# Optimization experiments

Measured on AMD Instinct MI355X. Metric: run time of the kernel, lower is better.

The kernel has to match this reference:

```python
import jax, jax.numpy as jnp
import numpy as np

N, E, F_IN, H0, H1 = 50000, 800000, 128, 128, 64


def setup_inputs() -> dict:
    key = jax.random.key(0)
    k1, k2, k3, k4, k5, k6 = jax.random.split(key, 6)
    node_features = jax.random.normal(k1, (N, F_IN), dtype=jnp.float32)
    edges = jax.random.randint(k2, (E, 2), 0, N, dtype=jnp.int64)
    # GCNConv params (glorot-ish scale)
    W1 = jax.random.normal(k3, (F_IN, H0), dtype=jnp.float32) / np.sqrt(F_IN)
    b1 = jnp.zeros((H0,), dtype=jnp.float32)
    W2 = jax.random.normal(k4, (H0, H1), dtype=jnp.float32) / np.sqrt(H0)
    b2 = jnp.zeros((H1,), dtype=jnp.float32)
    return {"node_features": node_features, "edges": edges,
            "W1": W1, "b1": b1, "W2": W2, "b2": b2}


def reference(node_features, edges, W1, b1, W2, b2):
    # GCNConv: out = D^{-1/2} (A + I) D^{-1/2} (X W) + b, with self-loops.
    n = node_features.shape[0]
    ei = edges.T  # [2, E] like edge_index.t() in the torch code
    self_idx = jnp.arange(n, dtype=ei.dtype)
    src = jnp.concatenate([ei[0], self_idx])  # [E+N]
    dst = jnp.concatenate([ei[1], self_idx])  # [E+N]
    deg = jnp.zeros((n,), node_features.dtype).at[dst].add(1.0)  # >=1 (self-loops)
    dinv = jax.lax.rsqrt(deg)
    norm = (dinv[src] * dinv[dst])[:, None]  # [E+N, 1]

    def gcn(x, W, b):
        h = x @ W                      # dense transform [n, d_out]
        msg = h[src] * norm            # gather + scale  [E+N, d_out]
        agg = jax.ops.segment_sum(msg, dst, num_segments=n)  # scatter-add
        return agg + b

    x = jax.nn.relu(gcn(node_features, W1, b1))
    # F.dropout(training=self.training): identity in eval mode (deterministic ref)
    x = gcn(x, W2, b2)
    return x
```

## Files before the change

kernel.cpp:

```cpp
#include <hip/hip_runtime.h>
#include <hip/hip_bf16.h>


#define NCHUNK 128

#define OFF_ROWSTART (size_t)0x0
#define OFF_DINV     (size_t)0x40000
#define OFF_BLOCKSUM (size_t)0x80000
#define OFF_FLAG     (size_t)0x80800
#define OFF_LRANK    (size_t)0x81000
#define OFF_CSR      (size_t)0x150000
#define OFF_H        (size_t)0x300000
#define OFF_W1T      (size_t)0xA00000
#define OFF_W2T      (size_t)0xA10000
#define OFF_BUFA     (size_t)0xB00000
#define OFF_BUFB     (size_t)0x1800000

typedef short bf16x8 __attribute__((ext_vector_type(8)));
typedef float f32x4 __attribute__((ext_vector_type(4)));

__device__ __forceinline__ float2 bf2f(unsigned u) {
    float2 r;
    r.x = __uint_as_float(u << 16);
    r.y = __uint_as_float(u & 0xffff0000u);
    return r;
}
__device__ __forceinline__ unsigned f2bf(float a, float b) {
    __hip_bfloat162 h = __float22bfloat162_rn(make_float2(a, b));
    union { __hip_bfloat162 h; unsigned u; } cv;
    cv.h = h;
    return cv.u;
}

__global__ __launch_bounds__(256) void k_hist(const int* __restrict__ e32, int E,
                                              int chunk, int n,
                                              unsigned char* __restrict__ lrank,
                                              unsigned char* __restrict__ H,
                                              int* __restrict__ flag,
                                              const float* __restrict__ W1,
                                              const float* __restrict__ W2,
                                              unsigned short* __restrict__ W1T,
                                              unsigned short* __restrict__ W2T) {
    const int t = threadIdx.x, b = blockIdx.x;
    if (b >= NCHUNK) {
        const int bb = b - NCHUNK;
        const int k0 = (t & 15) * 8;
        if (bb < 8) {
            int nn = bb * 16 + (t >> 4);
            float w[8];
#pragma unroll
            for (int j = 0; j < 8; ++j) w[j] = W1[(size_t)(k0 + j) * 128 + nn];
            uint4 q;
            q.x = f2bf(w[0], w[1]); q.y = f2bf(w[2], w[3]);
            q.z = f2bf(w[4], w[5]); q.w = f2bf(w[6], w[7]);
            *reinterpret_cast<uint4*>(&W1T[(size_t)nn * 128 + k0]) = q;
        } else {
            int nn = (bb - 8) * 16 + (t >> 4);
            float w[8];
#pragma unroll
            for (int j = 0; j < 8; ++j) w[j] = W2[(size_t)(k0 + j) * 64 + nn];
            uint4 q;
            q.x = f2bf(w[0], w[1]); q.y = f2bf(w[2], w[3]);
            q.z = f2bf(w[4], w[5]); q.w = f2bf(w[6], w[7]);
            *reinterpret_cast<uint4*>(&W2T[(size_t)nn * 128 + k0]) = q;
        }
        return;
    }
    __shared__ unsigned h[12544];
    __shared__ int anyv;
    const int nw = (n + 3) >> 2;
    if (t == 0) anyv = 0;
    for (int i = t; i < nw; i += 256) h[i] = 0u;
    __syncthreads();
    const int e0 = b * chunk, e1 = min(E, e0 + chunk);
    int v = 0;
    const int lim = min(e1, e0 + 2048);
    for (int e = e0 + t; e < lim; e += 256) v |= e32[2 * e + 1];
    if (v) atomicOr(&anyv, 1);
    __syncthreads();
    const int f = (anyv == 0) ? 1 : 0;
    if (b == 0 && t == 0) *flag = f;
    for (int e = e0 + t; e < e1; e += 256) {
        int dst;
        if (f) dst = reinterpret_cast<const int4*>(e32)[e].z;
        else   dst = reinterpret_cast<const int2*>(e32)[e].y;
        int sh = (dst & 3) << 3;
        unsigned old = atomicAdd(&h[dst >> 2], 1u << sh);
        lrank[e] = (unsigned char)((old >> sh) & 0xffu);
    }
    __syncthreads();
    unsigned* Hp = reinterpret_cast<unsigned*>(H);
    const size_t wbase = (size_t)b * (size_t)(n >> 2);
    for (int i = t; i < (n >> 2); i += 256) Hp[wbase + i] = h[i];
}

__global__ __launch_bounds__(256) void k_mergescan(
        unsigned char* __restrict__ H, int n,
        float* __restrict__ dinv, int* __restrict__ rowstart,
        int* __restrict__ blocksum) {
    __shared__ int sh[256];
    const int t = threadIdx.x;
    const int bin0 = blockIdx.x * 1024 + 4 * t;
    int s0 = 0, s1 = 0, s2 = 0, s3 = 0;
    if (bin0 < n) {
        unsigned* Hp = reinterpret_cast<unsigned*>(H);
        const size_t wstride = (size_t)(n >> 2);
        const size_t widx = (size_t)(bin0 >> 2);
#pragma unroll 8
        for (int b = 0; b < NCHUNK; ++b) {
            size_t idx = (size_t)b * wstride + widx;
            unsigned w = Hp[idx];
            Hp[idx] = (unsigned)s0 | ((unsigned)s1 << 8) |
                      ((unsigned)s2 << 16) | ((unsigned)s3 << 24);
            s0 += (int)(w & 0xffu);
            s1 += (int)((w >> 8) & 0xffu);
            s2 += (int)((w >> 16) & 0xffu);
            s3 += (int)((w >> 24) & 0xffu);
        }
        float4 dv;
        dv.x = rsqrtf((float)s0 + 1.0f);
        dv.y = rsqrtf((float)s1 + 1.0f);
        dv.z = rsqrtf((float)s2 + 1.0f);
        dv.w = rsqrtf((float)s3 + 1.0f);
        *reinterpret_cast<float4*>(dinv + bin0) = dv;
    }
    int tot = s0 + s1 + s2 + s3;
    sh[t] = tot;
    __syncthreads();
    for (int off = 1; off < 256; off <<= 1) {
        int add = (t >= off) ? sh[t - off] : 0;
        __syncthreads();
        sh[t] += add;
        __syncthreads();
    }
    if (bin0 < n) {
        int ex = sh[t] - tot;
        int4 rs;
        rs.x = ex;
        rs.y = ex + s0;
        rs.z = ex + s0 + s1;
        rs.w = ex + s0 + s1 + s2;
        *reinterpret_cast<int4*>(rowstart + bin0) = rs;
    }
    if (t == 255) blocksum[blockIdx.x] = sh[255];
}

__global__ void k_scan3(int* __restrict__ rowstart, int n,
                        const int* __restrict__ blocksum, int nb, int E) {
    __shared__ int bs[65];
    int t = threadIdx.x;
    if (t < nb) bs[t + 1] = blocksum[t];
    if (t == 0) bs[0] = 0;
    __syncthreads();
    if (t == 0) {
        int s = 0;
        for (int k = 1; k <= nb; ++k) { s += bs[k]; bs[k] = s; }
    }
    __syncthreads();
    int i = blockIdx.x * 256 + t;
    if (i < n) rowstart[i] += bs[i >> 10];
    if (i == 0) rowstart[n] = E;
}

__global__ __launch_bounds__(256) void k_fill(const int* __restrict__ e32, int E,
                                              int chunk,
                                              const int* __restrict__ flag,
                                              const int* __restrict__ rowstart,
                                              const unsigned char* __restrict__ H,
                                              int n,
                                              const unsigned char* __restrict__ lrank,
                                              unsigned short* __restrict__ csr) {
    __shared__ unsigned char hs[50176];
    const int t = threadIdx.x;
    const int b = blockIdx.x >> 1;
    const int half = blockIdx.x & 1;
    {
        const uint4* src = reinterpret_cast<const uint4*>(H + (size_t)b * n);
        uint4* dst = reinterpret_cast<uint4*>(hs);
        for (int i = t; i < (n >> 4); i += 256) dst[i] = src[i];
    }
    __syncthreads();
    const int f = *flag;
    const int hchunk = chunk >> 1;
    const int e0 = b * chunk + half * hchunk;
    const int e1 = min(E, e0 + hchunk);
    for (int e = e0 + t; e < e1; e += 256) {
        int src, dst;
        if (f) { int4 v = reinterpret_cast<const int4*>(e32)[e]; src = v.x; dst = v.z; }
        else   { int2 v = reinterpret_cast<const int2*>(e32)[e]; src = v.x; dst = v.y; }
        csr[rowstart[dst] + (int)hs[dst] + (int)lrank[e]] = (unsigned short)src;
    }
}

__global__ __launch_bounds__(256) void k_gemm1m(const float* __restrict__ X,
                                                const unsigned short* __restrict__ W1T,
                                                const float* __restrict__ dinv,
                                                unsigned short* __restrict__ out,
                                                int n) {
    __shared__ unsigned short Xs[64 * 136];
    __shared__ unsigned short Ws[128 * 136];
    const int t = threadIdx.x;
    const int row0 = blockIdx.x * 64;
#pragma unroll
    for (int it = 0; it < 8; ++it) {
        int i = t + it * 256;
        int r = i >> 4, c8 = i & 15;
        *reinterpret_cast<uint4*>(&Ws[r * 136 + c8 * 8]) =
            *reinterpret_cast<const uint4*>(&W1T[(size_t)r * 128 + c8 * 8]);
    }
#pragma unroll
    for (int it = 0; it < 8; ++it) {
        int i = t + it * 256;
        int r = i >> 5, c4 = i & 31;
        int gr = row0 + r;
        float4 v = make_float4(0.f, 0.f, 0.f, 0.f);
        if (gr < n) v = *reinterpret_cast<const float4*>(&X[(size_t)gr * 128 + c4 * 4]);
        uint2 q;
        q.x = f2bf(v.x, v.y);
        q.y = f2bf(v.z, v.w);
        *reinterpret_cast<uint2*>(&Xs[r * 136 + c4 * 4]) = q;
    }
    __syncthreads();
    const int w = t >> 6, lane = t & 63;
    const int m = lane & 15, kg = lane >> 4;
    f32x4 acc[8] = {};
#pragma unroll
    for (int kt = 0; kt < 128; kt += 32) {
        bf16x8 a = *reinterpret_cast<const bf16x8*>(&Xs[(w * 16 + m) * 136 + kt + kg * 8]);
#pragma unroll
        for (int j = 0; j < 8; ++j) {
            bf16x8 bb = *reinterpret_cast<const bf16x8*>(&Ws[(j * 16 + m) * 136 + kt + kg * 8]);
            acc[j] = __builtin_amdgcn_mfma_f32_16x16x32_bf16(a, bb, acc[j], 0, 0, 0);
        }
    }
    const int rbase = row0 + w * 16 + kg * 4;
#pragma unroll
    for (int r = 0; r < 4; ++r) {
        int gr = rbase + r;
        if (gr < n) {
            float dv = dinv[gr];
#pragma unroll
            for (int j = 0; j < 8; ++j)
                out[(size_t)gr * 128 + j * 16 + m] =
                    (unsigned short)(f2bf(acc[j][r] * dv, 0.f) & 0xffffu);
        }
    }
}

__global__ __launch_bounds__(256) void k_gemm2m(const unsigned short* __restrict__ X1,
                                                const unsigned short* __restrict__ W2T,
                                                const float* __restrict__ dinv,
                                                unsigned short* __restrict__ out,
                                                int n) {
    __shared__ unsigned short Xs[64 * 136];
    __shared__ unsigned short Ws[64 * 136];
    const int t = threadIdx.x;
    const int row0 = blockIdx.x * 64;
#pragma unroll
    for (int it = 0; it < 4; ++it) {
        int i = t + it * 256;
        int r = i >> 4, c8 = i & 15;
        *reinterpret_cast<uint4*>(&Ws[r * 136 + c8 * 8]) =
            *reinterpret_cast<const uint4*>(&W2T[(size_t)r * 128 + c8 * 8]);
    }
#pragma unroll
    for (int it = 0; it < 4; ++it) {
        int i = t + it * 256;
        int r = i >> 4, c8 = i & 15;
        int gr = row0 + r;
        uint4 q = make_uint4(0u, 0u, 0u, 0u);
        if (gr < n) q = *reinterpret_cast<const uint4*>(&X1[(size_t)gr * 128 + c8 * 8]);
        *reinterpret_cast<uint4*>(&Xs[r * 136 + c8 * 8]) = q;
    }
    __syncthreads();
    const int w = t >> 6, lane = t & 63;
    const int m = lane & 15, kg = lane >> 4;
    f32x4 acc[4] = {};
#pragma unroll
    for (int kt = 0; kt < 128; kt += 32) {
        bf16x8 a = *reinterpret_cast<const bf16x8*>(&Xs[(w * 16 + m) * 136 + kt + kg * 8]);
#pragma unroll
        for (int j = 0; j < 4; ++j) {
            bf16x8 bb = *reinterpret_cast<const bf16x8*>(&Ws[(j * 16 + m) * 136 + kt + kg * 8]);
            acc[j] = __builtin_amdgcn_mfma_f32_16x16x32_bf16(a, bb, acc[j], 0, 0, 0);
        }
    }
    const int rbase = row0 + w * 16 + kg * 4;
#pragma unroll
    for (int r = 0; r < 4; ++r) {
        int gr = rbase + r;
        if (gr < n) {
            float dv = dinv[gr];
#pragma unroll
            for (int j = 0; j < 4; ++j)
                out[(size_t)gr * 64 + j * 16 + m] =
                    (unsigned short)(f2bf(acc[j][r] * dv, 0.f) & 0xffffu);
        }
    }
}

__global__ __launch_bounds__(256) void k_spmm128h(
        const unsigned* __restrict__ H32, const int* __restrict__ rowstart,
        const unsigned short* __restrict__ csr, const float* __restrict__ dinv,
        const float* __restrict__ bias, unsigned* __restrict__ out, int n,
        int foff) {
    int node = blockIdx.x * 16 + (threadIdx.x >> 4);
    if (node >= n) return;
    int fq = (foff >> 2) + (threadIdx.x & 15);
    const uint2* H2 = reinterpret_cast<const uint2*>(H32);
    float di = dinv[node];
    uint2 sv = H2[(size_t)node * 32 + fq];
    float2 a0 = bf2f(sv.x), a1 = bf2f(sv.y);
    float acc0 = a0.x, acc1 = a0.y, acc2 = a1.x, acc3 = a1.y;
    int s0 = rowstart[node], s1 = rowstart[node + 1];
    for (int j = s0; j < s1; j += 8) {
        int srcs[8];
        uint2 uu[8];
#pragma unroll
        for (int u = 0; u < 8; ++u) srcs[u] = csr[min(j + u, s1 - 1)];
#pragma unroll
        for (int u = 0; u < 8; ++u) uu[u] = H2[(size_t)srcs[u] * 32 + fq];
#pragma unroll
        for (int u = 0; u < 8; ++u) {
            float2 f0 = bf2f(uu[u].x), f1 = bf2f(uu[u].y);
            bool ok = (j + u) < s1;
            acc0 += ok ? f0.x : 0.f;
            acc1 += ok ? f0.y : 0.f;
            acc2 += ok ? f1.x : 0.f;
            acc3 += ok ? f1.y : 0.f;
        }
    }
    float4 b = reinterpret_cast<const float4*>(bias)[fq];
    float o0 = fmaxf(fmaf(di, acc0, b.x), 0.f);
    float o1 = fmaxf(fmaf(di, acc1, b.y), 0.f);
    float o2 = fmaxf(fmaf(di, acc2, b.z), 0.f);
    float o3 = fmaxf(fmaf(di, acc3, b.w), 0.f);
    uint2 q;
    q.x = f2bf(o0, o1);
    q.y = f2bf(o2, o3);
    reinterpret_cast<uint2*>(out)[(size_t)node * 32 + fq] = q;
}

__global__ __launch_bounds__(256) void k_spmm64(
        const unsigned* __restrict__ H32, const int* __restrict__ rowstart,
        const unsigned short* __restrict__ csr, const float* __restrict__ dinv,
        const float* __restrict__ bias, float* __restrict__ out, int n) {
    int node = blockIdx.x * 16 + (threadIdx.x >> 4);
    if (node >= n) return;
    int f2 = threadIdx.x & 15;
    const uint2* H2 = reinterpret_cast<const uint2*>(H32);
    float di = dinv[node];
    uint2 sv = H2[(size_t)node * 16 + f2];
    float2 a0 = bf2f(sv.x), a1 = bf2f(sv.y);
    float acc0 = a0.x, acc1 = a0.y, acc2 = a1.x, acc3 = a1.y;
    int s0 = rowstart[node], s1 = rowstart[node + 1];
    for (int j = s0; j < s1; j += 8) {
        int srcs[8];
        uint2 uu[8];
#pragma unroll
        for (int u = 0; u < 8; ++u) srcs[u] = csr[min(j + u, s1 - 1)];
#pragma unroll
        for (int u = 0; u < 8; ++u) uu[u] = H2[(size_t)srcs[u] * 16 + f2];
#pragma unroll
        for (int u = 0; u < 8; ++u) {
            float2 f0 = bf2f(uu[u].x), f1 = bf2f(uu[u].y);
            bool ok = (j + u) < s1;
            acc0 += ok ? f0.x : 0.f;
            acc1 += ok ? f0.y : 0.f;
            acc2 += ok ? f1.x : 0.f;
            acc3 += ok ? f1.y : 0.f;
        }
    }
    float4 b = reinterpret_cast<const float4*>(bias)[f2];
    float4 o;
    o.x = fmaf(di, acc0, b.x);
    o.y = fmaf(di, acc1, b.y);
    o.z = fmaf(di, acc2, b.z);
    o.w = fmaf(di, acc3, b.w);
    reinterpret_cast<float4*>(out)[(size_t)node * 16 + f2] = o;
}

extern "C" void kernel_launch(void* const* d_in, const int* in_sizes, int n_in,
                              void* d_out, int out_size, void* d_ws, size_t ws_size,
                              hipStream_t stream) {
    const float* X   = (const float*)d_in[0];
    const int*   e32 = (const int*)d_in[1];
    const float* W1  = (const float*)d_in[2];
    const float* b1  = (const float*)d_in[3];
    const float* W2  = (const float*)d_in[4];
    const float* b2  = (const float*)d_in[5];
    float* out = (float*)d_out;

    const int n = in_sizes[0] / 128;
    const int E = in_sizes[1] / 2;
    const int chunk = (((E + NCHUNK - 1) / NCHUNK) + 511) & ~511;

    char* ws = (char*)d_ws;
    int*            rowstart = (int*)(ws + OFF_ROWSTART);
    float*          dinv     = (float*)(ws + OFF_DINV);
    int*            blocksum = (int*)(ws + OFF_BLOCKSUM);
    int*            flag     = (int*)(ws + OFF_FLAG);
    unsigned char*  lrank    = (unsigned char*)(ws + OFF_LRANK);
    unsigned short* csr      = (unsigned short*)(ws + OFF_CSR);
    unsigned char*  H        = (unsigned char*)(ws + OFF_H);
    unsigned short* W1T      = (unsigned short*)(ws + OFF_W1T);
    unsigned short* W2T      = (unsigned short*)(ws + OFF_W2T);
    unsigned short* bufA     = (unsigned short*)(ws + OFF_BUFA);
    unsigned*       bufB     = (unsigned*)(ws + OFF_BUFB);

    const int NB   = (n + 255) / 256;
    const int NBms = (n + 1023) / 1024;
    const int RB   = (n + 63) / 64;

    k_hist<<<NCHUNK + 12, 256, 0, stream>>>(e32, E, chunk, n, lrank, H, flag,
                                            W1, W2, W1T, W2T);
    k_mergescan<<<NBms, 256, 0, stream>>>(H, n, dinv, rowstart, blocksum);
    k_scan3<<<NB, 256, 0, stream>>>(rowstart, n, blocksum, NBms, E);
    k_fill<<<NCHUNK * 2, 256, 0, stream>>>(e32, E, chunk, flag, rowstart, H, n,
                                           lrank, csr);

    k_gemm1m<<<RB, 256, 0, stream>>>(X, W1T, dinv, bufA, n);
    k_spmm128h<<<(n + 15) / 16, 256, 0, stream>>>((const unsigned*)bufA, rowstart,
                                                  csr, dinv, b1, bufB, n, 0);
    k_spmm128h<<<(n + 15) / 16, 256, 0, stream>>>((const unsigned*)bufA, rowstart,
                                                  csr, dinv, b1, bufB, n, 64);
    k_gemm2m<<<RB, 256, 0, stream>>>((const unsigned short*)bufB, W2T, dinv, bufA, n);
    k_spmm64<<<(n + 15) / 16, 256, 0, stream>>>((const unsigned*)bufA, rowstart, csr,
                                                dinv, b2, out, n);
}
```

Baseline: 129.5 us.

## Pack edges in histogram pass and merge two half-width SpMM launches

The histogram kernel now writes each edge as a packed 32-bit (src16|dst16) word. The fill kernel reads that compact array instead of re-reading the int64 edge list and the layout flag, which cuts its edge-read traffic. The first-layer SpMM, previously two launches each covering half the 128 features, becomes one launch with 32 lanes per node covering all features, so the CSR indices are read once instead of twice. The cost is an extra 3.2 MB write in the histogram pass, and the packing assumes node ids fit in 16 bits.

```diff
diff --git a/kernel.cpp b/kernel.cpp
--- a/kernel.cpp
+++ b/kernel.cpp
@@ -15,6 +15,7 @@
 #define OFF_W2T      (size_t)0xA10000
 #define OFF_BUFA     (size_t)0xB00000
 #define OFF_BUFB     (size_t)0x1800000
+#define OFF_EPK      (size_t)0x2500000
 
 typedef short bf16x8 __attribute__((ext_vector_type(8)));
 typedef float f32x4 __attribute__((ext_vector_type(4)));
@@ -36,7 +37,7 @@
                                               int chunk, int n,
                                               unsigned char* __restrict__ lrank,
                                               unsigned char* __restrict__ H,
-                                              int* __restrict__ flag,
+                                              unsigned* __restrict__ epk,
                                               const float* __restrict__ W1,
                                               const float* __restrict__ W2,
                                               unsigned short* __restrict__ W1T,
@@ -79,11 +80,11 @@
     if (v) atomicOr(&anyv, 1);
     __syncthreads();
     const int f = (anyv == 0) ? 1 : 0;
-    if (b == 0 && t == 0) *flag = f;
     for (int e = e0 + t; e < e1; e += 256) {
-        int dst;
-        if (f) dst = reinterpret_cast<const int4*>(e32)[e].z;
-        else   dst = reinterpret_cast<const int2*>(e32)[e].y;
+        int src, dst;
+        if (f) { int4 w = reinterpret_cast<const int4*>(e32)[e]; src = w.x; dst = w.z; }
+        else   { int2 w = reinterpret_cast<const int2*>(e32)[e]; src = w.x; dst = w.y; }
+        epk[e] = (unsigned)src | ((unsigned)dst << 16);
         int sh = (dst & 3) << 3;
         unsigned old = atomicAdd(&h[dst >> 2], 1u << sh);
         lrank[e] = (unsigned char)((old >> sh) & 0xffu);
@@ -162,9 +163,8 @@
     if (i == 0) rowstart[n] = E;
 }
 
-__global__ __launch_bounds__(256) void k_fill(const int* __restrict__ e32, int E,
-                                              int chunk,
-                                              const int* __restrict__ flag,
+__global__ __launch_bounds__(256) void k_fill(const unsigned* __restrict__ epk,
+                                              int E, int chunk,
                                               const int* __restrict__ rowstart,
                                               const unsigned char* __restrict__ H,
                                               int n,
@@ -180,14 +180,13 @@
         for (int i = t; i < (n >> 4); i += 256) dst[i] = src[i];
     }
     __syncthreads();
-    const int f = *flag;
     const int hchunk = chunk >> 1;
     const int e0 = b * chunk + half * hchunk;
     const int e1 = min(E, e0 + hchunk);
     for (int e = e0 + t; e < e1; e += 256) {
-        int src, dst;
-        if (f) { int4 v = reinterpret_cast<const int4*>(e32)[e]; src = v.x; dst = v.z; }
-        else   { int2 v = reinterpret_cast<const int2*>(e32)[e]; src = v.x; dst = v.y; }
+        unsigned v = epk[e];
+        int src = (int)(v & 0xffffu);
+        int dst = (int)(v >> 16);
         csr[rowstart[dst] + (int)hs[dst] + (int)lrank[e]] = (unsigned short)src;
     }
 }
@@ -299,17 +298,16 @@
     }
 }
 
-__global__ __launch_bounds__(256) void k_spmm128h(
+__global__ __launch_bounds__(256) void k_spmm128(
         const unsigned* __restrict__ H32, const int* __restrict__ rowstart,
         const unsigned short* __restrict__ csr, const float* __restrict__ dinv,
-        const float* __restrict__ bias, unsigned* __restrict__ out, int n,
-        int foff) {
-    int node = blockIdx.x * 16 + (threadIdx.x >> 4);
+        const float* __restrict__ bias, unsigned* __restrict__ out, int n) {
+    int node = blockIdx.x * 8 + (threadIdx.x >> 5);
     if (node >= n) return;
-    int fq = (foff >> 2) + (threadIdx.x & 15);
+    int f2 = threadIdx.x & 31;
     const uint2* H2 = reinterpret_cast<const uint2*>(H32);
     float di = dinv[node];
-    uint2 sv = H2[(size_t)node * 32 + fq];
+    uint2 sv = H2[(size_t)node * 32 + f2];
     float2 a0 = bf2f(sv.x), a1 = bf2f(sv.y);
     float acc0 = a0.x, acc1 = a0.y, acc2 = a1.x, acc3 = a1.y;
     int s0 = rowstart[node], s1 = rowstart[node + 1];
@@ -319,7 +317,7 @@
 #pragma unroll
         for (int u = 0; u < 8; ++u) srcs[u] = csr[min(j + u, s1 - 1)];
 #pragma unroll
-        for (int u = 0; u < 8; ++u) uu[u] = H2[(size_t)srcs[u] * 32 + fq];
+        for (int u = 0; u < 8; ++u) uu[u] = H2[(size_t)srcs[u] * 32 + f2];
 #pragma unroll
         for (int u = 0; u < 8; ++u) {
             float2 f0 = bf2f(uu[u].x), f1 = bf2f(uu[u].y);
@@ -330,7 +328,7 @@
             acc3 += ok ? f1.y : 0.f;
         }
     }
-    float4 b = reinterpret_cast<const float4*>(bias)[fq];
+    float4 b = reinterpret_cast<const float4*>(bias)[f2];
     float o0 = fmaxf(fmaf(di, acc0, b.x), 0.f);
     float o1 = fmaxf(fmaf(di, acc1, b.y), 0.f);
     float o2 = fmaxf(fmaf(di, acc2, b.z), 0.f);
@@ -338,7 +336,7 @@
     uint2 q;
     q.x = f2bf(o0, o1);
     q.y = f2bf(o2, o3);
-    reinterpret_cast<uint2*>(out)[(size_t)node * 32 + fq] = q;
+    reinterpret_cast<uint2*>(out)[(size_t)node * 32 + f2] = q;
 }
 
 __global__ __launch_bounds__(256) void k_spmm64(
@@ -399,7 +397,6 @@
     int*            rowstart = (int*)(ws + OFF_ROWSTART);
     float*          dinv     = (float*)(ws + OFF_DINV);
     int*            blocksum = (int*)(ws + OFF_BLOCKSUM);
-    int*            flag     = (int*)(ws + OFF_FLAG);
     unsigned char*  lrank    = (unsigned char*)(ws + OFF_LRANK);
     unsigned short* csr      = (unsigned short*)(ws + OFF_CSR);
     unsigned char*  H        = (unsigned char*)(ws + OFF_H);
@@ -407,23 +404,22 @@
     unsigned short* W2T      = (unsigned short*)(ws + OFF_W2T);
     unsigned short* bufA     = (unsigned short*)(ws + OFF_BUFA);
     unsigned*       bufB     = (unsigned*)(ws + OFF_BUFB);
+    unsigned*       epk      = (unsigned*)(ws + OFF_EPK);
 
     const int NB   = (n + 255) / 256;
     const int NBms = (n + 1023) / 1024;
     const int RB   = (n + 63) / 64;
 
-    k_hist<<<NCHUNK + 12, 256, 0, stream>>>(e32, E, chunk, n, lrank, H, flag,
+    k_hist<<<NCHUNK + 12, 256, 0, stream>>>(e32, E, chunk, n, lrank, H, epk,
                                             W1, W2, W1T, W2T);
     k_mergescan<<<NBms, 256, 0, stream>>>(H, n, dinv, rowstart, blocksum);
     k_scan3<<<NB, 256, 0, stream>>>(rowstart, n, blocksum, NBms, E);
-    k_fill<<<NCHUNK * 2, 256, 0, stream>>>(e32, E, chunk, flag, rowstart, H, n,
+    k_fill<<<NCHUNK * 2, 256, 0, stream>>>(epk, E, chunk, rowstart, H, n,
                                            lrank, csr);
 
     k_gemm1m<<<RB, 256, 0, stream>>>(X, W1T, dinv, bufA, n);
-    k_spmm128h<<<(n + 15) / 16, 256, 0, stream>>>((const unsigned*)bufA, rowstart,
-                                                  csr, dinv, b1, bufB, n, 0);
-    k_spmm128h<<<(n + 15) / 16, 256, 0, stream>>>((const unsigned*)bufA, rowstart,
-                                                  csr, dinv, b1, bufB, n, 64);
+    k_spmm128<<<(n + 7) / 8, 256, 0, stream>>>((const unsigned*)bufA, rowstart, csr,
+                                               dinv, b1, bufB, n);
     k_gemm2m<<<RB, 256, 0, stream>>>((const unsigned short*)bufB, W2T, dinv, bufA, n);
     k_spmm64<<<(n + 15) / 16, 256, 0, stream>>>((const unsigned*)bufA, rowstart, csr,
                                                 dinv, b2, out, n);
```

After: 125.9 us (median of 2 runs). 2.8% less time.
